# Kernel tuning notes

Hardware: AMD Instinct MI355X
Metric: run time of the kernel (lower is better)

The kernel has to match this reference:

```python
import jax, jax.numpy as jnp
import numpy as np

BS, S, D, N, E = 16, 8, 10, 32, 300
H, STATE_DIM, MID, OC = 128, 96, 256, 100

def setup_inputs():
    ks = jax.random.split(jax.random.key(0), 24)
    g = lambda i, shape: (0.02 * jax.random.normal(ks[i], shape)).astype(jnp.float32)
    return {
        "stock_news": jax.random.normal(ks[0], (BS, S, D, N, E), dtype=jnp.float32),
        "stock_feats": jax.random.normal(ks[1], (BS, STATE_DIM), dtype=jnp.float32),
        "conv_w3": g(2, (S, OC, E, 3)), "conv_b3": g(3, (S, OC)),
        "conv_w4": g(4, (S, OC, E, 4)), "conv_b4": g(5, (S, OC)),
        "conv_w5": g(6, (S, OC, E, 5)), "conv_b5": g(7, (S, OC)),
        "w_ih": g(8, (S, 4 * H, 3 * OC)), "w_hh": g(9, (S, 4 * H, H)),
        "b_ih": g(10, (S, 4 * H)), "b_hh": g(11, (S, 4 * H)),
        "linX_w": g(12, (S, H, 2 * H)), "linX_b": g(13, (S, H)),
        "linY_w": g(14, (S, 64, H)), "linY_b": g(15, (S, 64)),
        "w1": g(16, (24, STATE_DIM)), "b1": g(17, (24,)),
        "w2": g(18, (16, 24)), "b2": g(19, (16,)),
        "arch_w1": g(20, (MID, 16 + 64 * S)), "arch_b1": g(21, (MID,)),
        "arch_w2": g(22, (S, MID)), "arch_b2": g(23, (S,)),
        "action_var": jnp.full((S,), -0.25, dtype=jnp.float32),
    }

def _conv_maxpool(x, w, b, k):
    # x: [S,B,D,N,E], w: [S,OC,E,k] -> conv1d over news axis then max-pool -> [S,B,D,OC]
    L = x.shape[3] - k + 1
    y = jnp.broadcast_to(b[:, None, None, None, :], (x.shape[0], x.shape[1], x.shape[2], L, w.shape[1]))
    for j in range(k):
        y = y + jnp.einsum('sbdne,soe->sbdno', x[:, :, :, j:j + L, :], w[:, :, :, j])
    return y.max(axis=3)

def _lstm_attn(xs, w_ih, w_hh, b_ih, b_hh):
    # single-stock LSTM (batch_first) + attention from original code; xs: [B,D,I] -> [B,2H]
    pre = jnp.einsum('bdi,gi->dbg', xs, w_ih) + b_ih + b_hh  # [D,B,4H]
    h0 = jnp.zeros((xs.shape[0], w_hh.shape[1]), xs.dtype)
    def step(carry, g_t):
        h, c = carry
        gates = g_t + h @ w_hh.T
        i, f, g, o = jnp.split(gates, 4, axis=-1)  # PyTorch gate order i,f,g,o
        c = jax.nn.sigmoid(f) * c + jax.nn.sigmoid(i) * jnp.tanh(g)
        h = jax.nn.sigmoid(o) * jnp.tanh(c)
        return (h, c), h
    (hn, _), outs = jax.lax.scan(step, (h0, h0), pre)
    outs = outs.transpose(1, 0, 2)  # [B,D,H]
    w = jnp.einsum('bh,bdh->bd', hn, outs)[:, None, :]  # [B,1,D]
    w = jax.nn.softmax(w, axis=1)  # softmax over singleton dim, exactly as torch code (yields ones)
    out = jnp.sum(w.transpose(0, 2, 1) * outs, axis=1)  # [B,H]
    return jnp.concatenate([hn, out], axis=-1)  # [B,2H]

def _forward(stock_news, stock_feats, conv_w3, conv_b3, conv_w4, conv_b4, conv_w5, conv_b5,
             w_ih, w_hh, b_ih, b_hh, linX_w, linX_b, linY_w, linY_b,
             w1, b1, w2, b2, arch_w1, arch_b1, arch_w2, arch_b2, action_var):
    x = stock_news.transpose(1, 0, 2, 3, 4)  # [S,B,D,N,E]
    feats = [_conv_maxpool(x, w, b, k) for (w, b, k) in
             ((conv_w3, conv_b3, 3), (conv_w4, conv_b4, 4), (conv_w5, conv_b5, 5))]
    text = jnp.concatenate(feats, axis=-1)  # [S,B,D,300]
    comb = jax.vmap(_lstm_attn)(text, w_ih, w_hh, b_ih, b_hh)  # [S,B,2H]
    hX = jax.nn.relu(jnp.einsum('sbi,shi->sbh', comb, linX_w) + linX_b[:, None, :])  # dropout is eval-mode identity
    hY = jax.nn.relu(jnp.einsum('sbh,soh->sbo', hX, linY_w) + linY_b[:, None, :])  # [S,B,64]
    stock_text = hY.transpose(1, 0, 2).reshape(stock_news.shape[0], -1)  # [B,S*64]
    f = jax.nn.relu(stock_feats @ w1.T + b1) @ w2.T + b2  # [B,16]
    total = jnp.concatenate([stock_text, f], axis=-1)  # [B,16+64S]
    mu = jnp.tanh(jax.nn.relu(total @ arch_w1.T + arch_b1) @ arch_w2.T + arch_b2)
    return mu, jnp.exp(action_var)

def reference(stock_news, stock_feats, conv_w3, conv_b3, conv_w4, conv_b4, conv_w5, conv_b5,
              w_ih, w_hh, b_ih, b_hh, linX_w, linX_b, linY_w, linY_b,
              w1, b1, w2, b2, arch_w1, arch_b1, arch_w2, arch_b2, action_var):
    return _forward(stock_news, stock_feats, conv_w3, conv_b3, conv_w4, conv_b4, conv_w5, conv_b5,
                    w_ih, w_hh, b_ih, b_hh, linX_w, linX_b, linY_w, linY_b,
                    w1, b1, w2, b2, arch_w1, arch_b1, arch_w2, arch_b2, action_var)
```

## Files before the change

### kernel.cpp

```cpp
#include <hip/hip_runtime.h>
#include <hip/hip_fp8.h>
#include <math.h>

#define S_   8
#define B_   16
#define D_   10
#define N_   32
#define E_   300
#define H_   128
#define G4_  512
#define SDIM_ 96
#define MID_ 256
#define TOT_ 528

typedef unsigned short u16;
typedef unsigned int u32;
typedef unsigned char u8;
typedef unsigned long long u64;
typedef __attribute__((ext_vector_type(8))) short short8;
typedef __attribute__((ext_vector_type(4))) float f32x4;

static __device__ __forceinline__ u16 f2bf(float f) {
    unsigned u = __builtin_bit_cast(unsigned, f);
    return (u16)((u + 0x7FFFu + ((u >> 16) & 1u)) >> 16);
}
static __device__ __forceinline__ u8 f2fp8(float f) {
    __hip_fp8_e4m3 t(f);
    return (u8)t.__x;
}

template<int KT>
static __device__ __forceinline__ void fill_row(const float* __restrict__ src,
                                                u8* __restrict__ tilerow, int lane) {
    const float4* s4 = reinterpret_cast<const float4*>(src);
    for (int i4 = lane; i4 < 75 * KT; i4 += 64) {
        float4 v = s4[i4];
        float vv[4] = {v.x, v.y, v.z, v.w};
#pragma unroll
        for (int k = 0; k < 4; ++k) {
            int p = i4 * 4 + k;
            int e = p / KT, tap = p - e * KT;
            tilerow[tap * 300 + e] = f2fp8(vv[k] * 16.0f);
        }
    }
}

__global__ __launch_bounds__(256) void prep(
        const float* __restrict__ w3, const float* __restrict__ b3,
        const float* __restrict__ w4, const float* __restrict__ b4,
        const float* __restrict__ w5, const float* __restrict__ b5,
        const float* __restrict__ w_ih,
        const float* __restrict__ lxw, const float* __restrict__ lyw,
        const float* __restrict__ aw1,
        u8* __restrict__ wpack3, u16* __restrict__ wpre2,
        float* __restrict__ bcomb,
        float* __restrict__ lxwT, float* __restrict__ lywT,
        float* __restrict__ aw1T) {
    const int blk = blockIdx.x, tid = threadIdx.x;

    if (blk < 640) {
        __shared__ u8 tile4[4][1504];
        const int s = blk / 80, cq = blk % 80;
        const int c0 = cq * 4;
        const int ch4 = tid >> 6, lane = tid & 63;
        for (int i = tid; i < 1504; i += 256)
            reinterpret_cast<u32*>(&tile4[0][0])[i] = 0u;
        __syncthreads();
        const int c = c0 + ch4;
        if (cq < 25)      fill_row<3>(w3 + (size_t)((s * 100 + c      ) * 300) * 3, &tile4[ch4][0], lane);
        else if (cq < 50) fill_row<4>(w4 + (size_t)((s * 100 + c - 100) * 300) * 4, &tile4[ch4][0], lane);
        else if (cq < 75) fill_row<5>(w5 + (size_t)((s * 100 + c - 200) * 300) * 5, &tile4[ch4][0], lane);
        __syncthreads();
        u32* dst0 = reinterpret_cast<u32*>(wpack3) + (size_t)s * 120320;
        const int kss = tid >> 5, m = tid & 31;
        const int ch = m >> 3, b0 = (m & 7) * 4;
#pragma unroll
        for (int ksb = 0; ksb < 6; ++ksb) {
            int ks = ksb * 8 + kss;
            if (ks < 47) {
                int kk = ks * 32 + b0;
                u32 v = (u32)tile4[ch][kk] | ((u32)tile4[ch][kk + 1] << 8)
                      | ((u32)tile4[ch][kk + 2] << 16) | ((u32)tile4[ch][kk + 3] << 24);
                dst0[(size_t)ks * 2560 + cq * 32 + m] = v;
            }
        }
    } else if (blk < 896) {
        __shared__ u16 tile2[16][320];
        const int u = blk - 640, s = u >> 5, gg = u & 31;
        const int ch = tid >> 4, lane = tid & 15;
        const int g = gg * 16 + ch;
        const float4* src4 = reinterpret_cast<const float4*>(w_ih + (size_t)(s * 512 + g) * 300);
        for (int i4 = lane; i4 < 75; i4 += 16) {
            float4 v = src4[i4];
            tile2[ch][i4 * 4 + 0] = f2bf(v.x); tile2[ch][i4 * 4 + 1] = f2bf(v.y);
            tile2[ch][i4 * 4 + 2] = f2bf(v.z); tile2[ch][i4 * 4 + 3] = f2bf(v.w);
        }
        for (int p = 300 + lane; p < 320; p += 16) tile2[ch][p] = 0;
        __syncthreads();
        u32* dst0 = reinterpret_cast<u32*>(wpre2 + (size_t)s * 163840 + gg * 512);
        const int mch = tid >> 4, rem = (tid * 2) & 31;
        for (int ks = 0; ks < 10; ++ks) {
            u32 v = (u32)tile2[mch][ks * 32 + rem] | ((u32)tile2[mch][ks * 32 + rem + 1] << 16);
            dst0[(size_t)ks * 8192 + tid] = v;
        }
    } else if (blk < 1352) {
        __shared__ float ldsT[32][33];
        const float* inp; float* outp;
        int inRS, outRS, i0, t0, ivalid = 32;
        if (blk < 1152) {
            int u = blk - 896, s = u >> 5, t32 = u & 31;
            int it = t32 >> 2, tt = t32 & 3;
            inp = lxw + (size_t)s * 128 * 256; outp = lxwT + (size_t)s * 256 * 128;
            inRS = 256; outRS = 128; i0 = it * 32; t0 = tt * 32;
        } else if (blk < 1216) {
            int u = blk - 1152, s = u >> 3, t32 = u & 7;
            int it = t32 >> 1, tt = t32 & 1;
            inp = lyw + (size_t)s * 64 * 128; outp = lywT + (size_t)s * 128 * 64;
            inRS = 128; outRS = 64; i0 = it * 32; t0 = tt * 32;
        } else {
            int u = blk - 1216;
            int it = u >> 3, jt = u & 7;
            inp = aw1; outp = aw1T;
            inRS = 528; outRS = 256; i0 = it * 32; t0 = jt * 32;
            ivalid = (i0 + 32 <= 528) ? 32 : (528 - i0);
        }
        const int row = tid >> 3, cf = tid & 7;
        float4 v = make_float4(0.f, 0.f, 0.f, 0.f);
        if (cf * 4 < ivalid)
            v = *reinterpret_cast<const float4*>(inp + (size_t)(t0 + row) * inRS + i0 + cf * 4);
        ldsT[cf * 4 + 0][row] = v.x; ldsT[cf * 4 + 1][row] = v.y;
        ldsT[cf * 4 + 2][row] = v.z; ldsT[cf * 4 + 3][row] = v.w;
        __syncthreads();
        if (row < ivalid) {
            float4 w;
            w.x = ldsT[row][cf * 4 + 0]; w.y = ldsT[row][cf * 4 + 1];
            w.z = ldsT[row][cf * 4 + 2]; w.w = ldsT[row][cf * 4 + 3];
            *reinterpret_cast<float4*>(outp + (size_t)(i0 + row) * outRS + t0 + cf * 4) = w;
        }
    } else {
        for (int i = tid; i < 2560; i += 256) {
            int c = i % 320, s = i / 320;
            float bv = 0.f;
            if (c < 100)      bv = b3[s*100 + c];
            else if (c < 200) bv = b4[s*100 + c - 100];
            else if (c < 300) bv = b5[s*100 + c - 200];
            bcomb[i] = bv;
        }
    }
}

__global__ __launch_bounds__(512, 1) void conv_mfma(const float* __restrict__ news,
                                                    const u8* __restrict__ wpack3,
                                                    const float* __restrict__ bcomb,
                                                    u16* __restrict__ text_bf) {
    __shared__ u8 xs[5 * 10816];
    __shared__ float part[10][320];
    const int tid = threadIdx.x, bid = blockIdx.x;
    const int s = bid & 7, rr_ = bid >> 3, b = rr_ >> 1, half = rr_ & 1;
    const int l = tid & 63, wvi = tid >> 6;
    const int wm = wvi >> 2, wn = wvi & 3;
    const int q = l >> 4, r16 = l & 15;

    const u8* gp[5];
#pragma unroll
    for (int nt = 0; nt < 5; ++nt) {
        int c = wn * 80 + nt * 16 + r16;
        gp[nt] = wpack3 + (size_t)s * 481280 + c * 32 + q * 8;
    }

    u64 bf0[5], bf1[5];
#pragma unroll
    for (int nt = 0; nt < 5; ++nt) bf0[nt] = *reinterpret_cast<const u64*>(gp[nt]);
#pragma unroll
    for (int nt = 0; nt < 5; ++nt) bf1[nt] = *reinterpret_cast<const u64*>(gp[nt] + 10240);

    {
        const float4* xg = reinterpret_cast<const float4*>(
            news + (size_t)((b * 8 + s) * 10 + half * 5) * 9600);
        for (int base = 0; base < 12000; base += 4096) {
            float4 v[8];
#pragma unroll
            for (int j = 0; j < 8; ++j) {
                int idx = base + j * 512 + tid;
                if (idx < 12000) v[j] = xg[idx];
            }
#pragma unroll
            for (int j = 0; j < 8; ++j) {
                int idx = base + j * 512 + tid;
                if (idx < 12000) {
                    int day = idx / 2400, rem = idx - day * 2400;
                    u32 o = (u32)f2fp8(v[j].x) | ((u32)f2fp8(v[j].y) << 8)
                          | ((u32)f2fp8(v[j].z) << 16) | ((u32)f2fp8(v[j].w) << 24);
                    *reinterpret_cast<u32*>(&xs[day * 10816 + rem * 4]) = o;
                }
            }
        }
        for (int i = tid; i < 1520; i += 512) {
            int day = i / 304, p = i - day * 304;
            *reinterpret_cast<u32*>(&xs[day * 10816 + 9600 + p * 4]) = 0u;
        }
    }
    __syncthreads();

    f32x4 acc[5][5];
#pragma unroll
    for (int mt = 0; mt < 5; ++mt)
#pragma unroll
        for (int nt = 0; nt < 5; ++nt) acc[mt][nt] = (f32x4)(0.f);

#define LOADA(dst, ks) do {                                                       \
    _Pragma("unroll")                                                             \
    for (int mt_ = 0; mt_ < 5; ++mt_) {                                           \
        int di_ = wm * 5 + mt_;                                                   \
        int off_ = (di_ >> 1) * 10816 + (((di_ & 1) << 4) + r16) * 300            \
                   + (ks) * 32 + q * 8;                                           \
        u32 lo_ = *reinterpret_cast<const u32*>(&xs[off_]);                       \
        u32 hi_ = *reinterpret_cast<const u32*>(&xs[off_ + 4]);                   \
        dst[mt_] = (u64)lo_ | ((u64)hi_ << 32);                                   \
    } } while (0)

#define MFMAS(bfv, av) do {                                                       \
    _Pragma("unroll")                                                             \
    for (int nt_ = 0; nt_ < 5; ++nt_)                                             \
        _Pragma("unroll")                                                         \
        for (int mt_ = 0; mt_ < 5; ++mt_)                                         \
            acc[mt_][nt_] = __builtin_amdgcn_mfma_f32_16x16x32_fp8_fp8(          \
                (long long)av[mt_], (long long)bfv[nt_], acc[mt_][nt_], 0, 0, 0); \
    } while (0)

    for (int ks = 0; ks < 46; ks += 2) {
        u64 a0[5], a1[5];
        LOADA(a0, ks);
        MFMAS(bf0, a0);
#pragma unroll
        for (int nt = 0; nt < 5; ++nt)
            bf0[nt] = *reinterpret_cast<const u64*>(gp[nt] + (ks + 2) * 10240);

        LOADA(a1, ks + 1);
        MFMAS(bf1, a1);
        if (ks + 3 < 47) {
#pragma unroll
            for (int nt = 0; nt < 5; ++nt)
                bf1[nt] = *reinterpret_cast<const u64*>(gp[nt] + (ks + 3) * 10240);
        }
    }
    {
        u64 a0[5];
        LOADA(a0, 46);
        MFMAS(bf0, a0);
    }
#undef LOADA
#undef MFMAS

#pragma unroll
    for (int mt = 0; mt < 5; ++mt) {
        const int di = wm * 5 + mt;
        const int nwb = (di & 1) << 4;
#pragma unroll
        for (int nt = 0; nt < 5; ++nt) {
            int oc = wn * 80 + nt * 16 + r16;
            int L = (oc < 100) ? 30 : (oc < 200) ? 29 : 28;
            float mx = -3e38f;
#pragma unroll
            for (int rr = 0; rr < 4; ++rr) {
                int nw = nwb + q * 4 + rr;
                if (nw < L) mx = fmaxf(mx, acc[mt][nt][rr]);
            }
            mx = fmaxf(mx, __shfl_xor(mx, 16));
            mx = fmaxf(mx, __shfl_xor(mx, 32));
            if (l < 16) part[di][wn * 80 + nt * 16 + l] = mx;
        }
    }
    __syncthreads();
    for (int i = tid; i < 1600; i += 512) {
        int day = i / 320, oc = i - day * 320;
        float mx = fmaxf(part[2 * day][oc], part[2 * day + 1][oc]);
        text_bf[((size_t)(s * 16 + b) * 10 + half * 5 + day) * 320 + oc] =
            f2bf(mx * 0.0625f + bcomb[s * 320 + oc]);
    }
}

__global__ __launch_bounds__(512) void stock_tail(const u16* __restrict__ text_bf,
                                                  const u16* __restrict__ wpre2,
                                                  const float* __restrict__ b_ih,
                                                  const float* __restrict__ b_hh,
                                                  const float* __restrict__ w_hh,
                                                  const float* __restrict__ lxwT, const float* __restrict__ lxb,
                                                  const float* __restrict__ lywT, const float* __restrict__ lyb,
                                                  float* __restrict__ total) {
    __shared__ u16 as16[16 * 320];
    __shared__ float pre_lds[D_][G4_];
    __shared__ float wchunk[128][129];
    __shared__ float h_lds[H_];
    __shared__ float gates[G4_];
    __shared__ float comb_l[256];
    __shared__ __align__(16) float hx[H_];
    const int sb = blockIdx.x;
    const int s = sb & 7, b = sb >> 3;
    const int t = threadIdx.x, l = t & 63, wv = t >> 6, q = l >> 4, r16 = l & 15;

    for (int i = t; i < 640; i += 512) {
        int r = i / 40, c = i % 40;
        float4 v = make_float4(0.f, 0.f, 0.f, 0.f);
        if (r < D_)
            v = *reinterpret_cast<const float4*>(
                text_bf + ((size_t)((s * 16 + b) * D_ + r)) * 320 + c * 8);
        *reinterpret_cast<float4*>(as16 + r * 320 + ((c ^ (r & 7)) << 3)) = v;
    }
    __syncthreads();

    {
        const u16* gpb[4];
#pragma unroll
        for (int nt = 0; nt < 4; ++nt) {
            int g = wv * 64 + nt * 16 + r16;
            gpb[nt] = wpre2 + (size_t)s * 163840 + g * 32 + q * 8;
        }
        f32x4 acc[4];
#pragma unroll
        for (int nt = 0; nt < 4; ++nt) acc[nt] = (f32x4)(0.f);
        for (int ks = 0; ks < 10; ++ks) {
            short8 a = *reinterpret_cast<const short8*>(
                as16 + r16 * 320 + (((ks * 4 + q) ^ (r16 & 7)) << 3));
#pragma unroll
            for (int nt = 0; nt < 4; ++nt) {
                short8 bf = *reinterpret_cast<const short8*>(gpb[nt] + ks * 16384);
                acc[nt] = __builtin_amdgcn_mfma_f32_16x16x32_bf16(a, bf, acc[nt], 0, 0, 0);
            }
        }
#pragma unroll
        for (int nt = 0; nt < 4; ++nt) {
            int g = wv * 64 + nt * 16 + r16;
            float bias = b_ih[s * G4_ + g] + b_hh[s * G4_ + g];
#pragma unroll
            for (int rr = 0; rr < 4; ++rr) {
                int row = q * 4 + rr;
                if (row < D_) pre_lds[row][g] = acc[nt][rr] + bias;
            }
        }
    }

    float wrs[128];
    for (int c = 0; c < 4; ++c) {
        __syncthreads();
        for (int i2 = t; i2 < 128 * 32; i2 += 512) {
            int row = i2 >> 5, fq = i2 & 31;
            float4 v = *reinterpret_cast<const float4*>(
                w_hh + ((size_t)(s * G4_ + c * 128 + row)) * H_ + fq * 4);
            wchunk[row][fq * 4 + 0] = v.x; wchunk[row][fq * 4 + 1] = v.y;
            wchunk[row][fq * 4 + 2] = v.z; wchunk[row][fq * 4 + 3] = v.w;
        }
        __syncthreads();
        if ((t >> 7) == c) {
            int r = t & 127;
#pragma unroll
            for (int i = 0; i < 128; ++i) wrs[i] = wchunk[r][i];
        }
    }
    __syncthreads();

    float cc = 0.f, hsum = 0.f, hval = 0.f;
    if (t < H_) h_lds[t] = 0.f;
    __syncthreads();

    for (int d = 0; d < D_; ++d) {
        float a0 = pre_lds[d][t];
        float a1 = 0.f, a2 = 0.f, a3 = 0.f;
#pragma unroll
        for (int i = 0; i < 128; i += 4) {
            float4 h4 = *reinterpret_cast<const float4*>(&h_lds[i]);
            a0 = fmaf(wrs[i + 0], h4.x, a0);
            a1 = fmaf(wrs[i + 1], h4.y, a1);
            a2 = fmaf(wrs[i + 2], h4.z, a2);
            a3 = fmaf(wrs[i + 3], h4.w, a3);
        }
        gates[t] = (a0 + a1) + (a2 + a3);
        __syncthreads();
        if (t < H_) {
            float ig = 1.f / (1.f + expf(-gates[t]));
            float fg = 1.f / (1.f + expf(-gates[H_ + t]));
            float gg = tanhf(gates[2 * H_ + t]);
            float og = 1.f / (1.f + expf(-gates[3 * H_ + t]));
            cc = fg * cc + ig * gg;
            hval = og * tanhf(cc);
            hsum += hval;
            h_lds[t] = hval;
        }
        __syncthreads();
    }
    if (t < H_) { comb_l[t] = hval; comb_l[H_ + t] = hsum; }
    __syncthreads();
    if (t < H_) {
        const float* wvp = lxwT + (size_t)s * 256 * 128 + t;
        float a0 = lxb[s * H_ + t], a1 = 0.f;
        for (int i = 0; i < 256; i += 2) {
            a0 = fmaf(comb_l[i], wvp[(size_t)i * 128], a0);
            a1 = fmaf(comb_l[i + 1], wvp[(size_t)(i + 1) * 128], a1);
        }
        hx[t] = fmaxf(a0 + a1, 0.f);
    }
    __syncthreads();
    if (t < 64) {
        const float* wvp = lywT + (size_t)s * 128 * 64 + t;
        float a0 = lyb[s * 64 + t], a1 = 0.f;
        for (int i = 0; i < 128; i += 2) {
            a0 = fmaf(hx[i], wvp[(size_t)i * 64], a0);
            a1 = fmaf(hx[i + 1], wvp[(size_t)(i + 1) * 64], a1);
        }
        total[(size_t)b * 512 + s * 64 + t] = fmaxf(a0 + a1, 0.f);
    }
}

__global__ __launch_bounds__(512) void head_feats(const float* __restrict__ total,
                                                  const float* __restrict__ sf,
                                                  const float* __restrict__ w1, const float* __restrict__ b1,
                                                  const float* __restrict__ w2, const float* __restrict__ b2,
                                                  const float* __restrict__ aw1T, const float* __restrict__ ab1,
                                                  const float* __restrict__ aw2, const float* __restrict__ ab2,
                                                  const float* __restrict__ avar,
                                                  float* __restrict__ out) {
    __shared__ __align__(16) float tr[TOT_];
    __shared__ float hid[MID_];
    __shared__ float h1f[24];
    __shared__ float pA[MID_], pB[MID_];
    const int bb = blockIdx.x, t = threadIdx.x;
    if (t < 128)
        reinterpret_cast<float4*>(tr)[t] = reinterpret_cast<const float4*>(total + (size_t)bb * 512)[t];
    if (t < 24) {
        float acc = b1[t];
        for (int i = 0; i < SDIM_; ++i) acc = fmaf(sf[bb * SDIM_ + i], w1[t * SDIM_ + i], acc);
        h1f[t] = fmaxf(acc, 0.f);
    }
    __syncthreads();
    if (t < 16) {
        float acc = b2[t];
        for (int i = 0; i < 24; ++i) acc = fmaf(h1f[i], w2[t * 24 + i], acc);
        tr[512 + t] = acc;
    }
    __syncthreads();
    {
        const int j = t & 255, hf = t >> 8;
        const int ilo = hf ? 264 : 0, ihi = hf ? 528 : 264;
        const float* wv = aw1T + j;
        float a0 = 0.f, a1 = 0.f, a2 = 0.f, a3 = 0.f;
        for (int i = ilo; i < ihi; i += 4) {
            a0 = fmaf(tr[i + 0], wv[(size_t)(i + 0) * 256], a0);
            a1 = fmaf(tr[i + 1], wv[(size_t)(i + 1) * 256], a1);
            a2 = fmaf(tr[i + 2], wv[(size_t)(i + 2) * 256], a2);
            a3 = fmaf(tr[i + 3], wv[(size_t)(i + 3) * 256], a3);
        }
        float p = (a0 + a1) + (a2 + a3);
        if (hf) pB[j] = p; else pA[j] = p;
    }
    __syncthreads();
    if (t < MID_) hid[t] = fmaxf(pA[t] + pB[t] + ab1[t], 0.f);
    __syncthreads();
    if (t < 8) {
        float acc = ab2[t];
        const float* wv = aw2 + (size_t)t * MID_;
        for (int i = 0; i < MID_; ++i) acc = fmaf(hid[i], wv[i], acc);
        out[bb * 8 + t] = tanhf(acc);
    }
    if (bb == 0 && t >= 8 && t < 16) out[128 + (t - 8)] = expf(avar[t - 8]);
}

extern "C" void kernel_launch(void* const* d_in, const int* in_sizes, int n_in,
                              void* d_out, int out_size, void* d_ws, size_t ws_size,
                              hipStream_t stream) {
    const float* news = (const float*)d_in[0];
    const float* sf   = (const float*)d_in[1];
    const float* w3   = (const float*)d_in[2];  const float* b3 = (const float*)d_in[3];
    const float* w4   = (const float*)d_in[4];  const float* b4 = (const float*)d_in[5];
    const float* w5   = (const float*)d_in[6];  const float* b5 = (const float*)d_in[7];
    const float* w_ih = (const float*)d_in[8];  const float* w_hh = (const float*)d_in[9];
    const float* b_ih = (const float*)d_in[10]; const float* b_hh = (const float*)d_in[11];
    const float* lxw  = (const float*)d_in[12]; const float* lxb = (const float*)d_in[13];
    const float* lyw  = (const float*)d_in[14]; const float* lyb = (const float*)d_in[15];
    const float* w1   = (const float*)d_in[16]; const float* b1 = (const float*)d_in[17];
    const float* w2   = (const float*)d_in[18]; const float* b2 = (const float*)d_in[19];
    const float* aw1  = (const float*)d_in[20]; const float* ab1 = (const float*)d_in[21];
    const float* aw2  = (const float*)d_in[22]; const float* ab2 = (const float*)d_in[23];
    const float* avar = (const float*)d_in[24];

    char* ws = (char*)d_ws;
    u8*    wpack3  = (u8*)ws;
    u16*   wpre2   = (u16*)(ws + 3850240);
    float* bcomb   = (float*)(ws + 6471680);
    u16*   text_bf = (u16*)(ws + 6481920);
    float* total   = (float*)(ws + 7301120);
    float* lxwT    = (float*)(ws + 7333888);
    float* lywT    = (float*)(ws + 8382464);
    float* aw1T    = (float*)(ws + 8644608);

    prep<<<1353, 256, 0, stream>>>(w3, b3, w4, b4, w5, b5, w_ih, lxw, lyw, aw1,
                                   wpack3, wpre2, bcomb, lxwT, lywT, aw1T);
    conv_mfma<<<256, 512, 0, stream>>>(news, wpack3, bcomb, text_bf);
    stock_tail<<<S_ * B_, 512, 0, stream>>>(text_bf, wpre2, b_ih, b_hh, w_hh,
                                            lxwT, lxb, lywT, lyb, total);
    head_feats<<<B_, 512, 0, stream>>>(total, sf, w1, b1, w2, b2, aw1T, ab1, aw2, ab2, avar, (float*)d_out);
}
```

Before: 110.0 us.

## Batch LSTM across batch per stock using bf16 MFMA for recurrent and linear layers

Restructures the LSTM tail so that one block handles all 16 batch rows of a stock, instead of one block per (stock, batch) pair. Every timestep now runs its input projection and its recurrent h@W_hh product as bf16 MFMA tiles, with the 16 batch rows forming the M dimension. The linX and linY layers also move to MFMA, and prep packs W_hh, linX and linY into bf16 MFMA layout in place of fp32 transposes. This removes the scalar per-thread 128-wide dot products and the redundant per-batch reloading of W_hh. The cost is only 8 blocks in flight, a recomputed input projection inside every step, and bf16 rounding of the hidden state and weights.

```diff
diff --git a/kernel.cpp b/kernel.cpp
--- a/kernel.cpp
+++ b/kernel.cpp
@@ -13,6 +13,8 @@
 #define MID_ 256
 #define TOT_ 528
 
+#define GP_  514
+
 typedef unsigned short u16;
 typedef unsigned int u32;
 typedef unsigned char u8;
@@ -49,13 +51,12 @@
         const float* __restrict__ w3, const float* __restrict__ b3,
         const float* __restrict__ w4, const float* __restrict__ b4,
         const float* __restrict__ w5, const float* __restrict__ b5,
-        const float* __restrict__ w_ih,
+        const float* __restrict__ w_ih, const float* __restrict__ w_hh,
         const float* __restrict__ lxw, const float* __restrict__ lyw,
         const float* __restrict__ aw1,
         u8* __restrict__ wpack3, u16* __restrict__ wpre2,
-        float* __restrict__ bcomb,
-        float* __restrict__ lxwT, float* __restrict__ lywT,
-        float* __restrict__ aw1T) {
+        u16* __restrict__ whh_pk, u16* __restrict__ lxw_pk, u16* __restrict__ lyw_pk,
+        float* __restrict__ bcomb, float* __restrict__ aw1T) {
     const int blk = blockIdx.x, tid = threadIdx.x;
 
     if (blk < 640) {
@@ -84,50 +85,73 @@
                 dst0[(size_t)ks * 2560 + cq * 32 + m] = v;
             }
         }
-    } else if (blk < 896) {
+    } else if (blk < 1248) {
         __shared__ u16 tile2[16][320];
-        const int u = blk - 640, s = u >> 5, gg = u & 31;
         const int ch = tid >> 4, lane = tid & 15;
-        const int g = gg * 16 + ch;
-        const float4* src4 = reinterpret_cast<const float4*>(w_ih + (size_t)(s * 512 + g) * 300);
-        for (int i4 = lane; i4 < 75; i4 += 16) {
-            float4 v = src4[i4];
-            tile2[ch][i4 * 4 + 0] = f2bf(v.x); tile2[ch][i4 * 4 + 1] = f2bf(v.y);
-            tile2[ch][i4 * 4 + 2] = f2bf(v.z); tile2[ch][i4 * 4 + 3] = f2bf(v.w);
-        }
-        for (int p = 300 + lane; p < 320; p += 16) tile2[ch][p] = 0;
-        __syncthreads();
-        u32* dst0 = reinterpret_cast<u32*>(wpre2 + (size_t)s * 163840 + gg * 512);
+        const float* src; u32* dst0; int nks, slab;
+        if (blk < 896) {
+            int u = blk - 640, s = u >> 5, gg = u & 31;
+            int g = gg * 16 + ch;
+            src = w_ih + (size_t)(s * 512 + g) * 300;
+            const float4* s4 = reinterpret_cast<const float4*>(src);
+            for (int i4 = lane; i4 < 75; i4 += 16) {
+                float4 v = s4[i4];
+                tile2[ch][i4*4+0]=f2bf(v.x); tile2[ch][i4*4+1]=f2bf(v.y);
+                tile2[ch][i4*4+2]=f2bf(v.z); tile2[ch][i4*4+3]=f2bf(v.w);
+            }
+            for (int p = 300 + lane; p < 320; p += 16) tile2[ch][p] = 0;
+            dst0 = reinterpret_cast<u32*>(wpre2 + (size_t)s * 163840) + gg * 256;
+            nks = 10; slab = 8192;
+        } else if (blk < 1152) {
+            int u = blk - 896, s = u >> 5, gg = u & 31;
+            int g = gg * 16 + ch;
+            const float4* s4 = reinterpret_cast<const float4*>(w_hh + (size_t)(s * 512 + g) * 128);
+            for (int i4 = lane; i4 < 32; i4 += 16) {
+                float4 v = s4[i4];
+                tile2[ch][i4*4+0]=f2bf(v.x); tile2[ch][i4*4+1]=f2bf(v.y);
+                tile2[ch][i4*4+2]=f2bf(v.z); tile2[ch][i4*4+3]=f2bf(v.w);
+            }
+            dst0 = reinterpret_cast<u32*>(whh_pk + (size_t)s * 65536) + gg * 256;
+            nks = 4; slab = 8192;
+        } else if (blk < 1216) {
+            int u = blk - 1152, s = u >> 3, gg = u & 7;
+            int g = gg * 16 + ch;
+            const float4* s4 = reinterpret_cast<const float4*>(lxw + (size_t)(s * 128 + g) * 256);
+            for (int i4 = lane; i4 < 64; i4 += 16) {
+                float4 v = s4[i4];
+                tile2[ch][i4*4+0]=f2bf(v.x); tile2[ch][i4*4+1]=f2bf(v.y);
+                tile2[ch][i4*4+2]=f2bf(v.z); tile2[ch][i4*4+3]=f2bf(v.w);
+            }
+            dst0 = reinterpret_cast<u32*>(lxw_pk + (size_t)s * 32768) + gg * 256;
+            nks = 8; slab = 2048;
+        } else {
+            int u = blk - 1216, s = u >> 2, gg = u & 3;
+            int g = gg * 16 + ch;
+            const float4* s4 = reinterpret_cast<const float4*>(lyw + (size_t)(s * 64 + g) * 128);
+            for (int i4 = lane; i4 < 32; i4 += 16) {
+                float4 v = s4[i4];
+                tile2[ch][i4*4+0]=f2bf(v.x); tile2[ch][i4*4+1]=f2bf(v.y);
+                tile2[ch][i4*4+2]=f2bf(v.z); tile2[ch][i4*4+3]=f2bf(v.w);
+            }
+            dst0 = reinterpret_cast<u32*>(lyw_pk + (size_t)s * 8192) + gg * 256;
+            nks = 4; slab = 1024;
+        }
+        __syncthreads();
         const int mch = tid >> 4, rem = (tid * 2) & 31;
-        for (int ks = 0; ks < 10; ++ks) {
+        for (int ks = 0; ks < nks; ++ks) {
             u32 v = (u32)tile2[mch][ks * 32 + rem] | ((u32)tile2[mch][ks * 32 + rem + 1] << 16);
-            dst0[(size_t)ks * 8192 + tid] = v;
-        }
-    } else if (blk < 1352) {
+            dst0[(size_t)ks * slab + tid] = v;
+        }
+    } else if (blk < 1384) {
         __shared__ float ldsT[32][33];
-        const float* inp; float* outp;
-        int inRS, outRS, i0, t0, ivalid = 32;
-        if (blk < 1152) {
-            int u = blk - 896, s = u >> 5, t32 = u & 31;
-            int it = t32 >> 2, tt = t32 & 3;
-            inp = lxw + (size_t)s * 128 * 256; outp = lxwT + (size_t)s * 256 * 128;
-            inRS = 256; outRS = 128; i0 = it * 32; t0 = tt * 32;
-        } else if (blk < 1216) {
-            int u = blk - 1152, s = u >> 3, t32 = u & 7;
-            int it = t32 >> 1, tt = t32 & 1;
-            inp = lyw + (size_t)s * 64 * 128; outp = lywT + (size_t)s * 128 * 64;
-            inRS = 128; outRS = 64; i0 = it * 32; t0 = tt * 32;
-        } else {
-            int u = blk - 1216;
-            int it = u >> 3, jt = u & 7;
-            inp = aw1; outp = aw1T;
-            inRS = 528; outRS = 256; i0 = it * 32; t0 = jt * 32;
-            ivalid = (i0 + 32 <= 528) ? 32 : (528 - i0);
-        }
+        int u = blk - 1248;
+        int it = u >> 3, jt = u & 7;
+        int i0 = it * 32, t0 = jt * 32;
+        int ivalid = (i0 + 32 <= 528) ? 32 : (528 - i0);
         const int row = tid >> 3, cf = tid & 7;
         float4 v = make_float4(0.f, 0.f, 0.f, 0.f);
         if (cf * 4 < ivalid)
-            v = *reinterpret_cast<const float4*>(inp + (size_t)(t0 + row) * inRS + i0 + cf * 4);
+            v = *reinterpret_cast<const float4*>(aw1 + (size_t)(t0 + row) * 528 + i0 + cf * 4);
         ldsT[cf * 4 + 0][row] = v.x; ldsT[cf * 4 + 1][row] = v.y;
         ldsT[cf * 4 + 2][row] = v.z; ldsT[cf * 4 + 3][row] = v.w;
         __syncthreads();
@@ -135,7 +159,7 @@
             float4 w;
             w.x = ldsT[row][cf * 4 + 0]; w.y = ldsT[row][cf * 4 + 1];
             w.z = ldsT[row][cf * 4 + 2]; w.w = ldsT[row][cf * 4 + 3];
-            *reinterpret_cast<float4*>(outp + (size_t)(i0 + row) * outRS + t0 + cf * 4) = w;
+            *reinterpret_cast<float4*>(aw1T + (size_t)(i0 + row) * 256 + t0 + cf * 4) = w;
         }
     } else {
         for (int i = tid; i < 2560; i += 256) {
@@ -280,134 +304,131 @@
     }
 }
 
-__global__ __launch_bounds__(512) void stock_tail(const u16* __restrict__ text_bf,
-                                                  const u16* __restrict__ wpre2,
-                                                  const float* __restrict__ b_ih,
-                                                  const float* __restrict__ b_hh,
-                                                  const float* __restrict__ w_hh,
-                                                  const float* __restrict__ lxwT, const float* __restrict__ lxb,
-                                                  const float* __restrict__ lywT, const float* __restrict__ lyb,
-                                                  float* __restrict__ total) {
-    __shared__ u16 as16[16 * 320];
-    __shared__ float pre_lds[D_][G4_];
-    __shared__ float wchunk[128][129];
-    __shared__ float h_lds[H_];
-    __shared__ float gates[G4_];
-    __shared__ float comb_l[256];
-    __shared__ __align__(16) float hx[H_];
-    const int sb = blockIdx.x;
-    const int s = sb & 7, b = sb >> 3;
+__global__ __launch_bounds__(512, 1) void stock_tail(const u16* __restrict__ text_bf,
+                                                     const u16* __restrict__ wpre2,
+                                                     const u16* __restrict__ whh_pk,
+                                                     const u16* __restrict__ lxw_pk,
+                                                     const u16* __restrict__ lyw_pk,
+                                                     const float* __restrict__ b_ih,
+                                                     const float* __restrict__ b_hh,
+                                                     const float* __restrict__ lxb,
+                                                     const float* __restrict__ lyb,
+                                                     float* __restrict__ total) {
+    __shared__ float gates[16 * GP_];
+    __shared__ u16 hA[16 * 128];
+    __shared__ u16 combA[16 * 256];
+    __shared__ u16 hxA[16 * 128];
+    const int s = blockIdx.x;
     const int t = threadIdx.x, l = t & 63, wv = t >> 6, q = l >> 4, r16 = l & 15;
 
-    for (int i = t; i < 640; i += 512) {
-        int r = i / 40, c = i % 40;
-        float4 v = make_float4(0.f, 0.f, 0.f, 0.f);
-        if (r < D_)
-            v = *reinterpret_cast<const float4*>(
-                text_bf + ((size_t)((s * 16 + b) * D_ + r)) * 320 + c * 8);
-        *reinterpret_cast<float4*>(as16 + r * 320 + ((c ^ (r & 7)) << 3)) = v;
-    }
-    __syncthreads();
-
-    {
-        const u16* gpb[4];
+    const u16 *gpre[4], *ghh[4];
+    float bias[4];
+#pragma unroll
+    for (int nt = 0; nt < 4; ++nt) {
+        int g = wv * 64 + nt * 16 + r16;
+        gpre[nt] = wpre2  + (size_t)s * 163840 + g * 32 + q * 8;
+        ghh[nt]  = whh_pk + (size_t)s * 65536  + g * 32 + q * 8;
+        bias[nt] = b_ih[s * G4_ + g] + b_hh[s * G4_ + g];
+    }
+    const u16* atext = text_bf + ((size_t)(s * 16 + r16) * 10) * 320 + q * 8;
+
+    reinterpret_cast<u64*>(hA)[t & 255] = 0ull;
+    float cst[4] = {0.f, 0.f, 0.f, 0.f};
+    float hsum[4] = {0.f, 0.f, 0.f, 0.f};
+    __syncthreads();
+
+    for (int d = 0; d < D_; ++d) {
+        f32x4 acc[4];
+#pragma unroll
+        for (int nt = 0; nt < 4; ++nt) acc[nt] = (f32x4)(bias[nt]);
+        const u16* ad = atext + d * 320;
+        for (int ks = 0; ks < 10; ++ks) {
+            short8 a = *reinterpret_cast<const short8*>(ad + ks * 32);
+#pragma unroll
+            for (int nt = 0; nt < 4; ++nt) {
+                short8 bfr = *reinterpret_cast<const short8*>(gpre[nt] + ks * 16384);
+                acc[nt] = __builtin_amdgcn_mfma_f32_16x16x32_bf16(a, bfr, acc[nt], 0, 0, 0);
+            }
+        }
+#pragma unroll
+        for (int ks2 = 0; ks2 < 4; ++ks2) {
+            int gran = (ks2 * 4 + q) ^ (r16 & 7);
+            short8 ah = *reinterpret_cast<const short8*>(&hA[r16 * 128 + gran * 8]);
+#pragma unroll
+            for (int nt = 0; nt < 4; ++nt) {
+                short8 bfr = *reinterpret_cast<const short8*>(ghh[nt] + ks2 * 16384);
+                acc[nt] = __builtin_amdgcn_mfma_f32_16x16x32_bf16(ah, bfr, acc[nt], 0, 0, 0);
+            }
+        }
+        __syncthreads();
 #pragma unroll
         for (int nt = 0; nt < 4; ++nt) {
             int g = wv * 64 + nt * 16 + r16;
-            gpb[nt] = wpre2 + (size_t)s * 163840 + g * 32 + q * 8;
-        }
-        f32x4 acc[4];
-#pragma unroll
-        for (int nt = 0; nt < 4; ++nt) acc[nt] = (f32x4)(0.f);
-        for (int ks = 0; ks < 10; ++ks) {
-            short8 a = *reinterpret_cast<const short8*>(
-                as16 + r16 * 320 + (((ks * 4 + q) ^ (r16 & 7)) << 3));
-#pragma unroll
-            for (int nt = 0; nt < 4; ++nt) {
-                short8 bf = *reinterpret_cast<const short8*>(gpb[nt] + ks * 16384);
-                acc[nt] = __builtin_amdgcn_mfma_f32_16x16x32_bf16(a, bf, acc[nt], 0, 0, 0);
-            }
-        }
-#pragma unroll
-        for (int nt = 0; nt < 4; ++nt) {
-            int g = wv * 64 + nt * 16 + r16;
-            float bias = b_ih[s * G4_ + g] + b_hh[s * G4_ + g];
-#pragma unroll
-            for (int rr = 0; rr < 4; ++rr) {
-                int row = q * 4 + rr;
-                if (row < D_) pre_lds[row][g] = acc[nt][rr] + bias;
-            }
-        }
-    }
-
-    float wrs[128];
-    for (int c = 0; c < 4; ++c) {
-        __syncthreads();
-        for (int i2 = t; i2 < 128 * 32; i2 += 512) {
-            int row = i2 >> 5, fq = i2 & 31;
-            float4 v = *reinterpret_cast<const float4*>(
-                w_hh + ((size_t)(s * G4_ + c * 128 + row)) * H_ + fq * 4);
-            wchunk[row][fq * 4 + 0] = v.x; wchunk[row][fq * 4 + 1] = v.y;
-            wchunk[row][fq * 4 + 2] = v.z; wchunk[row][fq * 4 + 3] = v.w;
-        }
-        __syncthreads();
-        if ((t >> 7) == c) {
-            int r = t & 127;
-#pragma unroll
-            for (int i = 0; i < 128; ++i) wrs[i] = wchunk[r][i];
-        }
-    }
-    __syncthreads();
-
-    float cc = 0.f, hsum = 0.f, hval = 0.f;
-    if (t < H_) h_lds[t] = 0.f;
-    __syncthreads();
-
-    for (int d = 0; d < D_; ++d) {
-        float a0 = pre_lds[d][t];
-        float a1 = 0.f, a2 = 0.f, a3 = 0.f;
-#pragma unroll
-        for (int i = 0; i < 128; i += 4) {
-            float4 h4 = *reinterpret_cast<const float4*>(&h_lds[i]);
-            a0 = fmaf(wrs[i + 0], h4.x, a0);
-            a1 = fmaf(wrs[i + 1], h4.y, a1);
-            a2 = fmaf(wrs[i + 2], h4.z, a2);
-            a3 = fmaf(wrs[i + 3], h4.w, a3);
-        }
-        gates[t] = (a0 + a1) + (a2 + a3);
-        __syncthreads();
-        if (t < H_) {
-            float ig = 1.f / (1.f + expf(-gates[t]));
-            float fg = 1.f / (1.f + expf(-gates[H_ + t]));
-            float gg = tanhf(gates[2 * H_ + t]);
-            float og = 1.f / (1.f + expf(-gates[3 * H_ + t]));
-            cc = fg * cc + ig * gg;
-            hval = og * tanhf(cc);
-            hsum += hval;
-            h_lds[t] = hval;
-        }
-        __syncthreads();
-    }
-    if (t < H_) { comb_l[t] = hval; comb_l[H_ + t] = hsum; }
-    __syncthreads();
-    if (t < H_) {
-        const float* wvp = lxwT + (size_t)s * 256 * 128 + t;
-        float a0 = lxb[s * H_ + t], a1 = 0.f;
-        for (int i = 0; i < 256; i += 2) {
-            a0 = fmaf(comb_l[i], wvp[(size_t)i * 128], a0);
-            a1 = fmaf(comb_l[i + 1], wvp[(size_t)(i + 1) * 128], a1);
-        }
-        hx[t] = fmaxf(a0 + a1, 0.f);
-    }
-    __syncthreads();
-    if (t < 64) {
-        const float* wvp = lywT + (size_t)s * 128 * 64 + t;
-        float a0 = lyb[s * 64 + t], a1 = 0.f;
-        for (int i = 0; i < 128; i += 2) {
-            a0 = fmaf(hx[i], wvp[(size_t)i * 64], a0);
-            a1 = fmaf(hx[i + 1], wvp[(size_t)(i + 1) * 64], a1);
-        }
-        total[(size_t)b * 512 + s * 64 + t] = fmaxf(a0 + a1, 0.f);
+#pragma unroll
+            for (int rr = 0; rr < 4; ++rr)
+                gates[(q * 4 + rr) * GP_ + g] = acc[nt][rr];
+        }
+        __syncthreads();
+#pragma unroll
+        for (int k = 0; k < 4; ++k) {
+            int p = t + 512 * k;
+            int b = p >> 7, h = p & 127;
+            float ig = 1.f / (1.f + expf(-gates[b * GP_ + h]));
+            float fg = 1.f / (1.f + expf(-gates[b * GP_ + 128 + h]));
+            float gg = tanhf(gates[b * GP_ + 256 + h]);
+            float og = 1.f / (1.f + expf(-gates[b * GP_ + 384 + h]));
+            float c = fg * cst[k] + ig * gg;
+            cst[k] = c;
+            float hv = og * tanhf(c);
+            hsum[k] += hv;
+            int swzg = (h >> 3) ^ (b & 7);
+            hA[b * 128 + swzg * 8 + (h & 7)] = f2bf(hv);
+            if (d == D_ - 1) {
+                int cg1 = (h >> 3) ^ (b & 7);
+                int cg2 = ((128 + h) >> 3) ^ (b & 7);
+                combA[b * 256 + cg1 * 8 + (h & 7)] = f2bf(hv);
+                combA[b * 256 + cg2 * 8 + (h & 7)] = f2bf(hsum[k]);
+            }
+        }
+        __syncthreads();
+    }
+
+    {
+        int col = wv * 16 + r16;
+        f32x4 xacc = (f32x4)(lxb[s * H_ + col]);
+        for (int ks = 0; ks < 8; ++ks) {
+            int gran = (ks * 4 + q) ^ (r16 & 7);
+            short8 a = *reinterpret_cast<const short8*>(&combA[r16 * 256 + gran * 8]);
+            short8 bfr = *reinterpret_cast<const short8*>(
+                lxw_pk + (size_t)s * 32768 + ks * 4096 + col * 32 + q * 8);
+            xacc = __builtin_amdgcn_mfma_f32_16x16x32_bf16(a, bfr, xacc, 0, 0, 0);
+        }
+#pragma unroll
+        for (int rr = 0; rr < 4; ++rr) {
+            int b = q * 4 + rr;
+            float v = fmaxf(xacc[rr], 0.f);
+            int swzg = (col >> 3) ^ (b & 7);
+            hxA[b * 128 + swzg * 8 + (col & 7)] = f2bf(v);
+        }
+    }
+    __syncthreads();
+
+    if (wv < 4) {
+        int col = wv * 16 + r16;
+        f32x4 yacc = (f32x4)(lyb[s * 64 + col]);
+#pragma unroll
+        for (int ks = 0; ks < 4; ++ks) {
+            int gran = (ks * 4 + q) ^ (r16 & 7);
+            short8 a = *reinterpret_cast<const short8*>(&hxA[r16 * 128 + gran * 8]);
+            short8 bfr = *reinterpret_cast<const short8*>(
+                lyw_pk + (size_t)s * 8192 + ks * 2048 + col * 32 + q * 8);
+            yacc = __builtin_amdgcn_mfma_f32_16x16x32_bf16(a, bfr, yacc, 0, 0, 0);
+        }
+#pragma unroll
+        for (int rr = 0; rr < 4; ++rr) {
+            int b = q * 4 + rr;
+            total[(size_t)b * 512 + s * 64 + col] = fmaxf(yacc[rr], 0.f);
+        }
     }
 }
 
@@ -485,17 +506,18 @@
     char* ws = (char*)d_ws;
     u8*    wpack3  = (u8*)ws;
     u16*   wpre2   = (u16*)(ws + 3850240);
-    float* bcomb   = (float*)(ws + 6471680);
-    u16*   text_bf = (u16*)(ws + 6481920);
-    float* total   = (float*)(ws + 7301120);
-    float* lxwT    = (float*)(ws + 7333888);
-    float* lywT    = (float*)(ws + 8382464);
-    float* aw1T    = (float*)(ws + 8644608);
-
-    prep<<<1353, 256, 0, stream>>>(w3, b3, w4, b4, w5, b5, w_ih, lxw, lyw, aw1,
-                                   wpack3, wpre2, bcomb, lxwT, lywT, aw1T);
+    u16*   whh_pk  = (u16*)(ws + 6471680);
+    u16*   lxw_pk  = (u16*)(ws + 7520256);
+    u16*   lyw_pk  = (u16*)(ws + 8044544);
+    float* bcomb   = (float*)(ws + 8175616);
+    u16*   text_bf = (u16*)(ws + 8185856);
+    float* total   = (float*)(ws + 9005056);
+    float* aw1T    = (float*)(ws + 9037824);
+
+    prep<<<1385, 256, 0, stream>>>(w3, b3, w4, b4, w5, b5, w_ih, w_hh, lxw, lyw, aw1,
+                                   wpack3, wpre2, whh_pk, lxw_pk, lyw_pk, bcomb, aw1T);
     conv_mfma<<<256, 512, 0, stream>>>(news, wpack3, bcomb, text_bf);
-    stock_tail<<<S_ * B_, 512, 0, stream>>>(text_bf, wpre2, b_ih, b_hh, w_hh,
-                                            lxwT, lxb, lywT, lyb, total);
+    stock_tail<<<S_, 512, 0, stream>>>(text_bf, wpre2, whh_pk, lxw_pk, lyw_pk,
+                                       b_ih, b_hh, lxb, lyb, total);
     head_feats<<<B_, 512, 0, stream>>>(total, sf, w1, b1, w2, b2, aw1T, ab1, aw2, ab2, avar, (float*)d_out);
 }
```

Result: slower. 185.1 us (+68.3%).
